# Optimization experiments

Hardware: AMD Instinct MI355X
Metric: run time of the kernel (lower is better)

The kernel has to match this reference:

```python
import jax, jax.numpy as jnp
import numpy as np

DIM = 1024
HEADS = 16
HEAD_DIM = DIM // HEADS
HIDDEN = 4 * DIM
B, N = 4, 2048


def _layernorm(x, g, b, eps=1e-5):
    mu = jnp.mean(x, axis=-1, keepdims=True)
    var = jnp.var(x, axis=-1, keepdims=True)
    return (x - mu) * jax.lax.rsqrt(var + eps) * g + b


def setup_inputs() -> dict:
    key = jax.random.key(0)
    ks = jax.random.split(key, 8)
    s_in = 1.0 / np.sqrt(DIM)
    s_hid = 1.0 / np.sqrt(HIDDEN)
    return {
        "x": jax.random.normal(ks[0], (B, N, DIM), jnp.float32),
        "w_qkv": jax.random.normal(ks[1], (DIM, 3 * DIM), jnp.float32) * s_in,
        "w_proj": jax.random.normal(ks[2], (DIM, DIM), jnp.float32) * s_in,
        "b_proj": jnp.zeros((DIM,), jnp.float32),
        "ln1_g": jnp.ones((DIM,), jnp.float32),
        "ln1_b": jnp.zeros((DIM,), jnp.float32),
        "w1": jax.random.normal(ks[3], (DIM, HIDDEN), jnp.float32) * s_in,
        "b1": jnp.zeros((HIDDEN,), jnp.float32),
        "w2": jax.random.normal(ks[4], (HIDDEN, DIM), jnp.float32) * s_hid,
        "b2": jnp.zeros((DIM,), jnp.float32),
        "ln2_g": jnp.ones((DIM,), jnp.float32),
        "ln2_b": jnp.zeros((DIM,), jnp.float32),
    }


def reference(x, w_qkv, w_proj, b_proj, ln1_g, ln1_b, w1, b1, w2, b2, ln2_g, ln2_b):
    # --- multi-head self-attention (pre-norm), dropout=0 (eval) ---
    h = _layernorm(x, ln1_g, ln1_b)
    qkv = h @ w_qkv                       # [B,N,3*DIM]
    qkv = qkv.reshape(B, N, 3, HEADS, HEAD_DIM)
    q = jnp.transpose(qkv[:, :, 0], (0, 2, 1, 3))  # [B,H,N,hd]
    k = jnp.transpose(qkv[:, :, 1], (0, 2, 1, 3))
    v = jnp.transpose(qkv[:, :, 2], (0, 2, 1, 3))
    scale = HEAD_DIM ** -0.5
    attn = jnp.einsum('bhqd,bhkd->bhqk', q, k) * scale  # [B,H,N,N]
    attn = jax.nn.softmax(attn, axis=-1)
    o = jnp.einsum('bhqk,bhkd->bhqd', attn, v)
    o = jnp.transpose(o, (0, 2, 1, 3)).reshape(B, N, DIM)
    x = o @ w_proj + b_proj + x
    # --- feed-forward (pre-norm), exact GELU ---
    h = _layernorm(x, ln2_g, ln2_b)
    h = jax.nn.gelu(h @ w1 + b1, approximate=False)
    return h @ w2 + b2 + x
```

## Files before the change

kernel.cpp:

```cpp
#include <hip/hip_runtime.h>
#include <cstdint>
#include <cstddef>

typedef float  v4f  __attribute__((ext_vector_type(4)));
typedef __bf16 v8bf __attribute__((ext_vector_type(8)));
typedef __bf16 v4bf __attribute__((ext_vector_type(4)));

__device__ __forceinline__ float b2f(unsigned short u) {
  union { unsigned int i; float f; } cv; cv.i = ((unsigned int)u) << 16; return cv.f;
}
__device__ __forceinline__ unsigned short f2b(float f) {
  union { float f; unsigned int i; } cv; cv.f = f;
  unsigned int i = cv.i;
  i += 0x7fffu + ((i >> 16) & 1u);
  return (unsigned short)(i >> 16);
}
__device__ __forceinline__ unsigned short f2b_trunc(float f) {
  union { float f; unsigned int i; } cv; cv.f = f;
  return (unsigned short)(cv.i >> 16);
}
__device__ __forceinline__ float gelu_fast(float x) {
  const float u = x * (1.5957691216f + 0.07135481627f * x * x);
  return x * (1.0f / (1.0f + __expf(-u)));
}
__device__ __forceinline__ void g2l16(const unsigned short* g, unsigned short* l) {
  __builtin_amdgcn_global_load_lds(
      (const __attribute__((address_space(1))) void*)g,
      (__attribute__((address_space(3))) void*)l,
      16, 0, 0);
}

__global__ __launch_bounds__(256) void transpose_k(const float* __restrict__ in,
                                                   unsigned short* __restrict__ out,
                                                   int R, int C) {
  __shared__ float tile[32][33];
  const int tx = threadIdx.x, ty = threadIdx.y;
  const int r0 = blockIdx.y * 32, c0 = blockIdx.x * 32;
#pragma unroll
  for (int j = 0; j < 4; ++j)
    tile[ty + 8 * j][tx] = in[(size_t)(r0 + ty + 8 * j) * C + c0 + tx];
  __syncthreads();
#pragma unroll
  for (int j = 0; j < 4; ++j)
    out[(size_t)(c0 + ty + 8 * j) * R + r0 + tx] = f2b(tile[tx][ty + 8 * j]);
}

__global__ __launch_bounds__(256) void ln_kernel(const void* __restrict__ xp, int in_bf16,
                                                 const float* __restrict__ g,
                                                 const float* __restrict__ bta,
                                                 unsigned short* __restrict__ out) {
  const int r = blockIdx.x, t = threadIdx.x;
  float v0, v1, v2, v3;
  if (in_bf16) {
    const ushort4 raw = *(const ushort4*)((const unsigned short*)xp + (size_t)r * 1024 + t * 4);
    v0 = b2f(raw.x); v1 = b2f(raw.y); v2 = b2f(raw.z); v3 = b2f(raw.w);
  } else {
    const float4 raw = *(const float4*)((const float*)xp + (size_t)r * 1024 + t * 4);
    v0 = raw.x; v1 = raw.y; v2 = raw.z; v3 = raw.w;
  }
  float s  = v0 + v1 + v2 + v3;
  float s2 = v0 * v0 + v1 * v1 + v2 * v2 + v3 * v3;
#pragma unroll
  for (int off = 32; off > 0; off >>= 1) {
    s  += __shfl_down(s, off);
    s2 += __shfl_down(s2, off);
  }
  __shared__ float red[8];
  const int w = t >> 6, lane = t & 63;
  if (lane == 0) { red[w] = s; red[4 + w] = s2; }
  __syncthreads();
  if (t == 0) {
    float ts = red[0] + red[1] + red[2] + red[3];
    float t2 = red[4] + red[5] + red[6] + red[7];
    float mu = ts * (1.0f / 1024.0f);
    float var = t2 * (1.0f / 1024.0f) - mu * mu;
    red[0] = mu;
    red[1] = rsqrtf(var + 1e-5f);
  }
  __syncthreads();
  const float mu = red[0], rs = red[1];
  const float4 graw = *(const float4*)(g + t * 4);
  const float4 braw = *(const float4*)(bta + t * 4);
  ushort4 o;
  o.x = f2b((v0 - mu) * rs * graw.x + braw.x);
  o.y = f2b((v1 - mu) * rs * graw.y + braw.y);
  o.z = f2b((v2 - mu) * rs * graw.z + braw.z);
  o.w = f2b((v3 - mu) * rs * graw.w + braw.w);
  *(ushort4*)(out + (size_t)r * 1024 + t * 4) = o;
}

__global__ __launch_bounds__(256, 2) void gemm_bt(const unsigned short* __restrict__ A,
                                                  const unsigned short* __restrict__ Bt,
                                                  const float* __restrict__ bias,
                                                  const void* __restrict__ res, int res_bf16,
                                                  void* __restrict__ Cout,
                                                  int M, int N, int K, int act, int out_bf16,
                                                  int swap_xy) {
  __shared__ __align__(16) unsigned short As[3][128 * 32];
  __shared__ __align__(16) unsigned short Bs[3][128 * 32];
  const int t = threadIdx.x;
  const int lane = t & 63, w = t >> 6;
  const int wr = (w >> 1) * 64, wc = (w & 1) * 64;
  const int lr = lane & 15, lq = lane >> 4;
  const int mb = swap_xy ? blockIdx.x : blockIdx.y;
  const int nb = swap_xy ? blockIdx.y : blockIdx.x;
  const int m0 = mb * 128, n0 = nb * 128;

  const int c0 = t, c1 = t + 256;
  const int r0 = c0 >> 2, o0 = (((c0 & 3) ^ ((c0 >> 3) & 3)) << 3);
  const int r1 = c1 >> 2, o1 = (((c1 & 3) ^ ((c1 >> 3) & 3)) << 3);
  const unsigned short* Ag0 = A  + (size_t)(m0 + r0) * K + o0;
  const unsigned short* Ag1 = A  + (size_t)(m0 + r1) * K + o1;
  const unsigned short* Bg0 = Bt + (size_t)(n0 + r0) * K + o0;
  const unsigned short* Bg1 = Bt + (size_t)(n0 + r1) * K + o1;

  const int ra = ((lq ^ ((lr >> 1) & 3)) << 3);

  v4f acc[4][4];
#pragma unroll
  for (int mi = 0; mi < 4; ++mi)
#pragma unroll
    for (int ni = 0; ni < 4; ++ni)
      acc[mi][ni] = (v4f){0.f, 0.f, 0.f, 0.f};

  const int nt = K >> 5;
  g2l16(Ag0, &As[0][c0 * 8]); g2l16(Bg0, &Bs[0][c0 * 8]);
  g2l16(Ag1, &As[0][c1 * 8]); g2l16(Bg1, &Bs[0][c1 * 8]);
  if (nt > 1) {
    g2l16(Ag0 + 32, &As[1][c0 * 8]); g2l16(Bg0 + 32, &Bs[1][c0 * 8]);
    g2l16(Ag1 + 32, &As[1][c1 * 8]); g2l16(Bg1 + 32, &Bs[1][c1 * 8]);
  }

  int bi = 0;
  for (int tt = 0; tt < nt; ++tt) {
    const int pf = tt + 2;
    if (pf < nt) {
      const int ko = pf << 5;
      const int pb = pf % 3;
      g2l16(Ag0 + ko, &As[pb][c0 * 8]); g2l16(Bg0 + ko, &Bs[pb][c0 * 8]);
      g2l16(Ag1 + ko, &As[pb][c1 * 8]); g2l16(Bg1 + ko, &Bs[pb][c1 * 8]);
      asm volatile("s_waitcnt vmcnt(8)" ::: "memory");
    } else if (tt + 1 < nt) {
      asm volatile("s_waitcnt vmcnt(4)" ::: "memory");
    } else {
      asm volatile("s_waitcnt vmcnt(0)" ::: "memory");
    }
    __builtin_amdgcn_s_barrier();
    asm volatile("" ::: "memory");

    v8bf af[4], bfr[4];
#pragma unroll
    for (int i = 0; i < 4; ++i) {
      af[i]  = *(const v8bf*)(&As[bi][(wr + i * 16 + lr) * 32 + ra]);
      bfr[i] = *(const v8bf*)(&Bs[bi][(wc + i * 16 + lr) * 32 + ra]);
    }
#pragma unroll
    for (int mi = 0; mi < 4; ++mi)
#pragma unroll
      for (int ni = 0; ni < 4; ++ni)
        acc[mi][ni] = __builtin_amdgcn_mfma_f32_16x16x32_bf16(af[mi], bfr[ni], acc[mi][ni], 0, 0, 0);

    asm volatile("" ::: "memory");
    __builtin_amdgcn_s_barrier();
    bi = (bi == 2) ? 0 : bi + 1;
  }

#pragma unroll
  for (int mi = 0; mi < 4; ++mi) {
#pragma unroll
    for (int ni = 0; ni < 4; ++ni) {
      const int col = n0 + wc + ni * 16 + lr;
      const float bv = bias ? bias[col] : 0.0f;
#pragma unroll
      for (int r = 0; r < 4; ++r) {
        const int row = m0 + wr + mi * 16 + lq * 4 + r;
        float v = acc[mi][ni][r] + bv;
        if (act) v = gelu_fast(v);
        if (res) {
          v += res_bf16 ? b2f(((const unsigned short*)res)[(size_t)row * N + col])
                        : ((const float*)res)[(size_t)row * N + col];
        }
        if (out_bf16)
          ((unsigned short*)Cout)[(size_t)row * N + col] = f2b(v);
        else
          ((float*)Cout)[(size_t)row * N + col] = v;
      }
    }
  }
}

__global__ __launch_bounds__(256) void vt_k(const unsigned short* __restrict__ qkv,
                                            unsigned short* __restrict__ Vt) {
  const int t = threadIdx.x;
  const int n = blockIdx.x * 256 + t, h = blockIdx.y, b = blockIdx.z;
  const size_t src = (size_t)(b * 2048 + n) * 3072 + 2048 + h * 64;
  unsigned short v[64];
#pragma unroll
  for (int j = 0; j < 8; ++j)
    *(uint4*)(v + j * 8) = *(const uint4*)(qkv + src + j * 8);
  const size_t dstbase = ((size_t)(b * 16 + h) * 64) * 2048 + n;
#pragma unroll
  for (int d = 0; d < 64; ++d)
    Vt[dstbase + (size_t)d * 2048] = v[d];
}

__global__ __launch_bounds__(256, 3) void attn_mfma(const unsigned short* __restrict__ qkv,
                                                    const unsigned short* __restrict__ Vt,
                                                    unsigned short* __restrict__ out) {
  __shared__ __align__(16) unsigned short Ks[64 * 80];
  __shared__ __align__(16) unsigned short Vs[64 * 80];
  __shared__ __align__(16) unsigned short Ps[4][32 * 76];
  const int t = threadIdx.x;
  const int lane = t & 63, w = t >> 6;
  const int lr = lane & 15, lq = lane >> 4;
  const int h = blockIdx.x, b = blockIdx.z;
  const int q0 = blockIdx.y * 128 + w * 32;

  v8bf aq[2][2];
#pragma unroll
  for (int mi = 0; mi < 2; ++mi)
#pragma unroll
    for (int kq = 0; kq < 2; ++kq) {
      aq[mi][kq] = *(const v8bf*)(qkv + (size_t)(b * 2048 + q0 + mi * 16 + lr) * 3072
                                  + h * 64 + kq * 32 + lq * 8);
#pragma unroll
      for (int j = 0; j < 8; ++j)
        aq[mi][kq][j] = (__bf16)((float)aq[mi][kq][j] * 0.125f);
    }

  v4f acc_o[2][4];
  float lsum[2][4];
#pragma unroll
  for (int mi = 0; mi < 2; ++mi)
#pragma unroll
    for (int di = 0; di < 4; ++di)
      acc_o[mi][di] = (v4f){0.f, 0.f, 0.f, 0.f};
#pragma unroll
  for (int mi = 0; mi < 2; ++mi)
#pragma unroll
    for (int r = 0; r < 4; ++r)
      lsum[mi][r] = 0.0f;

  const int sc0 = t, sc1 = t + 256;
  const int kr0 = sc0 >> 3, ko0 = (sc0 & 7) * 8;
  const int kr1 = sc1 >> 3, ko1 = (sc1 & 7) * 8;
  const unsigned short* Kg0 = qkv + (size_t)(b * 2048 + kr0) * 3072 + 1024 + h * 64 + ko0;
  const unsigned short* Kg1 = qkv + (size_t)(b * 2048 + kr1) * 3072 + 1024 + h * 64 + ko1;
  const unsigned short* Vg0 = Vt + ((size_t)(b * 16 + h) * 64 + kr0) * 2048 + ko0;
  const unsigned short* Vg1 = Vt + ((size_t)(b * 16 + h) * 64 + kr1) * 2048 + ko1;

  uint4 kreg0 = *(const uint4*)(Kg0);
  uint4 kreg1 = *(const uint4*)(Kg1);
  uint4 vreg0 = *(const uint4*)(Vg0);
  uint4 vreg1 = *(const uint4*)(Vg1);
  *(uint4*)(Ks + kr0 * 80 + ko0) = kreg0;
  *(uint4*)(Ks + kr1 * 80 + ko1) = kreg1;
  *(uint4*)(Vs + kr0 * 80 + ko0) = vreg0;
  *(uint4*)(Vs + kr1 * 80 + ko1) = vreg1;
  __syncthreads();

  for (int kt = 0; kt < 32; ++kt) {
    if (kt < 31) {
      const size_t kn = (size_t)(kt + 1) * 64;
      kreg0 = *(const uint4*)(Kg0 + kn * 3072);
      kreg1 = *(const uint4*)(Kg1 + kn * 3072);
      vreg0 = *(const uint4*)(Vg0 + kn);
      vreg1 = *(const uint4*)(Vg1 + kn);
    }

    v4f s_acc[2][4];
#pragma unroll
    for (int mi = 0; mi < 2; ++mi)
#pragma unroll
      for (int ni = 0; ni < 4; ++ni)
        s_acc[mi][ni] = (v4f){0.f, 0.f, 0.f, 0.f};
#pragma unroll
    for (int kq = 0; kq < 2; ++kq) {
      v8bf bk[4];
#pragma unroll
      for (int ni = 0; ni < 4; ++ni)
        bk[ni] = *(const v8bf*)(Ks + (ni * 16 + lr) * 80 + kq * 32 + lq * 8);
      __builtin_amdgcn_s_setprio(1);
#pragma unroll
      for (int mi = 0; mi < 2; ++mi)
#pragma unroll
        for (int ni = 0; ni < 4; ++ni)
          s_acc[mi][ni] = __builtin_amdgcn_mfma_f32_16x16x32_bf16(aq[mi][kq], bk[ni], s_acc[mi][ni], 0, 0, 0);
      __builtin_amdgcn_s_setprio(0);
    }

#pragma unroll
    for (int mi = 0; mi < 2; ++mi)
#pragma unroll
      for (int ni = 0; ni < 4; ++ni)
#pragma unroll
        for (int r = 0; r < 4; ++r) {
          const float p = __expf(s_acc[mi][ni][r]);
          const unsigned short pb = f2b_trunc(p);
          lsum[mi][r] += b2f(pb);
          Ps[w][(mi * 16 + lq * 4 + r) * 76 + ni * 16 + lr] = pb;
        }

#pragma unroll
    for (int ks = 0; ks < 2; ++ks) {
      v8bf ap[2], bv[4];
#pragma unroll
      for (int mi = 0; mi < 2; ++mi) {
        const unsigned short* base = Ps[w] + (mi * 16 + lr) * 76 + ks * 32 + lq * 8;
        const v4bf lo = *(const v4bf*)(base);
        const v4bf hi = *(const v4bf*)(base + 4);
        ap[mi] = __builtin_shufflevector(lo, hi, 0, 1, 2, 3, 4, 5, 6, 7);
      }
#pragma unroll
      for (int di = 0; di < 4; ++di)
        bv[di] = *(const v8bf*)(Vs + (di * 16 + lr) * 80 + ks * 32 + lq * 8);
      __builtin_amdgcn_s_setprio(1);
#pragma unroll
      for (int mi = 0; mi < 2; ++mi)
#pragma unroll
        for (int di = 0; di < 4; ++di)
          acc_o[mi][di] = __builtin_amdgcn_mfma_f32_16x16x32_bf16(ap[mi], bv[di], acc_o[mi][di], 0, 0, 0);
      __builtin_amdgcn_s_setprio(0);
    }

    __syncthreads();
    if (kt < 31) {
      *(uint4*)(Ks + kr0 * 80 + ko0) = kreg0;
      *(uint4*)(Ks + kr1 * 80 + ko1) = kreg1;
      *(uint4*)(Vs + kr0 * 80 + ko0) = vreg0;
      *(uint4*)(Vs + kr1 * 80 + ko1) = vreg1;
    }
    __syncthreads();
  }

#pragma unroll
  for (int mi = 0; mi < 2; ++mi)
#pragma unroll
    for (int r = 0; r < 4; ++r) {
      float v = lsum[mi][r];
      v += __shfl_xor(v, 1);
      v += __shfl_xor(v, 2);
      v += __shfl_xor(v, 4);
      v += __shfl_xor(v, 8);
      lsum[mi][r] = 1.0f / v;
    }

#pragma unroll
  for (int mi = 0; mi < 2; ++mi)
#pragma unroll
    for (int di = 0; di < 4; ++di)
#pragma unroll
      for (int r = 0; r < 4; ++r)
        out[(size_t)(b * 2048 + q0 + mi * 16 + lq * 4 + r) * 1024 + h * 64 + di * 16 + lr] =
            f2b(acc_o[mi][di][r] * lsum[mi][r]);
}

extern "C" void kernel_launch(void* const* d_in, const int* in_sizes, int n_in,
                              void* d_out, int out_size, void* d_ws, size_t ws_size,
                              hipStream_t stream) {
  (void)in_sizes; (void)n_in; (void)out_size; (void)ws_size;
  const float* x      = (const float*)d_in[0];
  const float* w_qkv  = (const float*)d_in[1];
  const float* w_proj = (const float*)d_in[2];
  const float* b_proj = (const float*)d_in[3];
  const float* ln1_g  = (const float*)d_in[4];
  const float* ln1_b  = (const float*)d_in[5];
  const float* w1     = (const float*)d_in[6];
  const float* b1     = (const float*)d_in[7];
  const float* w2     = (const float*)d_in[8];
  const float* b2     = (const float*)d_in[9];
  const float* ln2_g  = (const float*)d_in[10];
  const float* ln2_b  = (const float*)d_in[11];
  float* out = (float*)d_out;

  char* ws = (char*)d_ws;
  unsigned short* T_a   = (unsigned short*)(ws);
  unsigned short* T_b   = (unsigned short*)(ws + 8388608);
  unsigned short* x2buf = (unsigned short*)(ws + 16777216);
  unsigned short* Vtbuf = (unsigned short*)(ws + 33554432);
  unsigned short* Hbuf  = (unsigned short*)(ws + 50331648);
  unsigned short* qkvb  = (unsigned short*)(ws + 67108864);
  unsigned short* h3buf = (unsigned short*)(ws + 50331648);
  unsigned short* h2buf = (unsigned short*)d_out;

  const dim3 tb(32, 8);
  transpose_k<<<dim3(96, 32),  tb, 0, stream>>>(w_qkv,  T_a, 1024, 3072);
  transpose_k<<<dim3(32, 32),  tb, 0, stream>>>(w_proj, T_b, 1024, 1024);
  ln_kernel<<<8192, 256, 0, stream>>>(x, 0, ln1_g, ln1_b, Hbuf);
  gemm_bt<<<dim3(24, 64), 256, 0, stream>>>(Hbuf, T_a, nullptr, nullptr, 0, qkvb, 8192, 3072, 1024, 0, 1, 0);
  transpose_k<<<dim3(128, 32), tb, 0, stream>>>(w1, T_a, 1024, 4096);
  vt_k<<<dim3(8, 16, 4), 256, 0, stream>>>(qkvb, Vtbuf);
  attn_mfma<<<dim3(16, 16, 4), 256, 0, stream>>>(qkvb, Vtbuf, Hbuf);
  gemm_bt<<<dim3(64, 8), 256, 0, stream>>>(Hbuf, T_b, b_proj, x, 0, x2buf, 8192, 1024, 1024, 0, 1, 1);
  transpose_k<<<dim3(32, 128), tb, 0, stream>>>(w2, T_b, 4096, 1024);
  ln_kernel<<<8192, 256, 0, stream>>>(x2buf, 1, ln2_g, ln2_b, h2buf);
  gemm_bt<<<dim3(32, 64), 256, 0, stream>>>(h2buf, T_a, b1, nullptr, 0, h3buf, 8192, 4096, 1024, 1, 1, 0);
  gemm_bt<<<dim3(64, 8), 256, 0, stream>>>(h3buf, T_b, b2, x2buf, 1, out, 8192, 1024, 4096, 0, 0, 1);
}
```

Measured before the change: 576.6 us.

## Fuse V transpose into QKV GEMM epilogue and double-buffer attention K/V tiles

Drops the separate V-transpose kernel: the QKV GEMM epilogue now also writes the V columns in transposed layout. The attention kernel double-buffers its K/V shared-memory tiles, which removes one barrier per iteration, and it lowers the occupancy hint from 3 to 2 blocks. The log2(e) factor is folded into the Q scale so softmax can call exp2f instead of __expf. The transposed V stores from the GEMM epilogue are scattered 2-byte writes, so that epilogue gets more expensive, and the larger shared-memory footprint can cut attention occupancy.

```diff
diff --git a/kernel.cpp b/kernel.cpp
--- a/kernel.cpp
+++ b/kernel.cpp
@@ -94,6 +94,7 @@
                                                   const float* __restrict__ bias,
                                                   const void* __restrict__ res, int res_bf16,
                                                   void* __restrict__ Cout,
+                                                  unsigned short* __restrict__ vt,
                                                   int M, int N, int K, int act, int out_bf16,
                                                   int swap_xy) {
   __shared__ __align__(16) unsigned short As[3][128 * 32];
@@ -184,31 +185,21 @@
           ((unsigned short*)Cout)[(size_t)row * N + col] = f2b(v);
         else
           ((float*)Cout)[(size_t)row * N + col] = v;
+        if (vt && col >= 2048) {
+          const int hh = (col - 2048) >> 6, dd = (col - 2048) & 63;
+          const int bb = row >> 11, nn = row & 2047;
+          vt[(((size_t)bb * 16 + hh) * 64 + dd) * 2048 + nn] = f2b(v);
+        }
       }
     }
   }
 }
 
-__global__ __launch_bounds__(256) void vt_k(const unsigned short* __restrict__ qkv,
-                                            unsigned short* __restrict__ Vt) {
-  const int t = threadIdx.x;
-  const int n = blockIdx.x * 256 + t, h = blockIdx.y, b = blockIdx.z;
-  const size_t src = (size_t)(b * 2048 + n) * 3072 + 2048 + h * 64;
-  unsigned short v[64];
-#pragma unroll
-  for (int j = 0; j < 8; ++j)
-    *(uint4*)(v + j * 8) = *(const uint4*)(qkv + src + j * 8);
-  const size_t dstbase = ((size_t)(b * 16 + h) * 64) * 2048 + n;
-#pragma unroll
-  for (int d = 0; d < 64; ++d)
-    Vt[dstbase + (size_t)d * 2048] = v[d];
-}
-
-__global__ __launch_bounds__(256, 3) void attn_mfma(const unsigned short* __restrict__ qkv,
+__global__ __launch_bounds__(256, 2) void attn_mfma(const unsigned short* __restrict__ qkv,
                                                     const unsigned short* __restrict__ Vt,
                                                     unsigned short* __restrict__ out) {
-  __shared__ __align__(16) unsigned short Ks[64 * 80];
-  __shared__ __align__(16) unsigned short Vs[64 * 80];
+  __shared__ __align__(16) unsigned short Ks[2][64 * 80];
+  __shared__ __align__(16) unsigned short Vs[2][64 * 80];
   __shared__ __align__(16) unsigned short Ps[4][32 * 76];
   const int t = threadIdx.x;
   const int lane = t & 63, w = t >> 6;
@@ -216,6 +207,7 @@
   const int h = blockIdx.x, b = blockIdx.z;
   const int q0 = blockIdx.y * 128 + w * 32;
 
+  const float qscale = 0.125f * 1.4426950408889634f;
   v8bf aq[2][2];
 #pragma unroll
   for (int mi = 0; mi < 2; ++mi)
@@ -225,7 +217,7 @@
                                   + h * 64 + kq * 32 + lq * 8);
 #pragma unroll
       for (int j = 0; j < 8; ++j)
-        aq[mi][kq][j] = (__bf16)((float)aq[mi][kq][j] * 0.125f);
+        aq[mi][kq][j] = (__bf16)((float)aq[mi][kq][j] * qscale);
     }
 
   v4f acc_o[2][4];
@@ -253,13 +245,14 @@
   uint4 kreg1 = *(const uint4*)(Kg1);
   uint4 vreg0 = *(const uint4*)(Vg0);
   uint4 vreg1 = *(const uint4*)(Vg1);
-  *(uint4*)(Ks + kr0 * 80 + ko0) = kreg0;
-  *(uint4*)(Ks + kr1 * 80 + ko1) = kreg1;
-  *(uint4*)(Vs + kr0 * 80 + ko0) = vreg0;
-  *(uint4*)(Vs + kr1 * 80 + ko1) = vreg1;
+  *(uint4*)(Ks[0] + kr0 * 80 + ko0) = kreg0;
+  *(uint4*)(Ks[0] + kr1 * 80 + ko1) = kreg1;
+  *(uint4*)(Vs[0] + kr0 * 80 + ko0) = vreg0;
+  *(uint4*)(Vs[0] + kr1 * 80 + ko1) = vreg1;
   __syncthreads();
 
   for (int kt = 0; kt < 32; ++kt) {
+    const int cur = kt & 1;
     if (kt < 31) {
       const size_t kn = (size_t)(kt + 1) * 64;
       kreg0 = *(const uint4*)(Kg0 + kn * 3072);
@@ -279,7 +272,7 @@
       v8bf bk[4];
 #pragma unroll
       for (int ni = 0; ni < 4; ++ni)
-        bk[ni] = *(const v8bf*)(Ks + (ni * 16 + lr) * 80 + kq * 32 + lq * 8);
+        bk[ni] = *(const v8bf*)(Ks[cur] + (ni * 16 + lr) * 80 + kq * 32 + lq * 8);
       __builtin_amdgcn_s_setprio(1);
 #pragma unroll
       for (int mi = 0; mi < 2; ++mi)
@@ -295,7 +288,7 @@
       for (int ni = 0; ni < 4; ++ni)
 #pragma unroll
         for (int r = 0; r < 4; ++r) {
-          const float p = __expf(s_acc[mi][ni][r]);
+          const float p = exp2f(s_acc[mi][ni][r]);
           const unsigned short pb = f2b_trunc(p);
           lsum[mi][r] += b2f(pb);
           Ps[w][(mi * 16 + lq * 4 + r) * 76 + ni * 16 + lr] = pb;
@@ -313,7 +306,7 @@
       }
 #pragma unroll
       for (int di = 0; di < 4; ++di)
-        bv[di] = *(const v8bf*)(Vs + (di * 16 + lr) * 80 + ks * 32 + lq * 8);
+        bv[di] = *(const v8bf*)(Vs[cur] + (di * 16 + lr) * 80 + ks * 32 + lq * 8);
       __builtin_amdgcn_s_setprio(1);
 #pragma unroll
       for (int mi = 0; mi < 2; ++mi)
@@ -323,12 +316,11 @@
       __builtin_amdgcn_s_setprio(0);
     }
 
-    __syncthreads();
     if (kt < 31) {
-      *(uint4*)(Ks + kr0 * 80 + ko0) = kreg0;
-      *(uint4*)(Ks + kr1 * 80 + ko1) = kreg1;
-      *(uint4*)(Vs + kr0 * 80 + ko0) = vreg0;
-      *(uint4*)(Vs + kr1 * 80 + ko1) = vreg1;
+      *(uint4*)(Ks[cur ^ 1] + kr0 * 80 + ko0) = kreg0;
+      *(uint4*)(Ks[cur ^ 1] + kr1 * 80 + ko1) = kreg1;
+      *(uint4*)(Vs[cur ^ 1] + kr0 * 80 + ko0) = vreg0;
+      *(uint4*)(Vs[cur ^ 1] + kr1 * 80 + ko1) = vreg1;
     }
     __syncthreads();
   }
@@ -387,13 +379,12 @@
   transpose_k<<<dim3(96, 32),  tb, 0, stream>>>(w_qkv,  T_a, 1024, 3072);
   transpose_k<<<dim3(32, 32),  tb, 0, stream>>>(w_proj, T_b, 1024, 1024);
   ln_kernel<<<8192, 256, 0, stream>>>(x, 0, ln1_g, ln1_b, Hbuf);
-  gemm_bt<<<dim3(24, 64), 256, 0, stream>>>(Hbuf, T_a, nullptr, nullptr, 0, qkvb, 8192, 3072, 1024, 0, 1, 0);
+  gemm_bt<<<dim3(24, 64), 256, 0, stream>>>(Hbuf, T_a, nullptr, nullptr, 0, qkvb, Vtbuf, 8192, 3072, 1024, 0, 1, 0);
   transpose_k<<<dim3(128, 32), tb, 0, stream>>>(w1, T_a, 1024, 4096);
-  vt_k<<<dim3(8, 16, 4), 256, 0, stream>>>(qkvb, Vtbuf);
   attn_mfma<<<dim3(16, 16, 4), 256, 0, stream>>>(qkvb, Vtbuf, Hbuf);
-  gemm_bt<<<dim3(64, 8), 256, 0, stream>>>(Hbuf, T_b, b_proj, x, 0, x2buf, 8192, 1024, 1024, 0, 1, 1);
+  gemm_bt<<<dim3(64, 8), 256, 0, stream>>>(Hbuf, T_b, b_proj, x, 0, x2buf, nullptr, 8192, 1024, 1024, 0, 1, 1);
   transpose_k<<<dim3(32, 128), tb, 0, stream>>>(w2, T_b, 4096, 1024);
   ln_kernel<<<8192, 256, 0, stream>>>(x2buf, 1, ln2_g, ln2_b, h2buf);
-  gemm_bt<<<dim3(32, 64), 256, 0, stream>>>(h2buf, T_a, b1, nullptr, 0, h3buf, 8192, 4096, 1024, 1, 1, 0);
-  gemm_bt<<<dim3(64, 8), 256, 0, stream>>>(h3buf, T_b, b2, x2buf, 1, out, 8192, 1024, 4096, 0, 0, 1);
-}
+  gemm_bt<<<dim3(32, 64), 256, 0, stream>>>(h2buf, T_a, b1, nullptr, 0, h3buf, nullptr, 8192, 4096, 1024, 1, 1, 0);
+  gemm_bt<<<dim3(64, 8), 256, 0, stream>>>(h3buf, T_b, b2, x2buf, 1, out, nullptr, 8192, 1024, 4096, 0, 0, 1);
+}
```

Result: slower. 619.2 us (+7.4%).
